# Kernel optimization log

Measured on AMD Instinct MI355X. Metric: run time of the kernel, lower is better.

## Reference

```python
import jax, jax.numpy as jnp
import numpy as np

N_NODES = 50000
N_EDGES = 800000
NUM_GRAPHS = 256
IN = 128
HID = 256
NUM_CLASSES = 10
EPS = 1e-5


def _glorot(key, shape):
    fan_in, fan_out = shape[0], shape[1]
    lim = (6.0 / (fan_in + fan_out)) ** 0.5
    return jax.random.uniform(key, shape, jnp.float32, -lim, lim)


def setup_inputs() -> dict:
    key = jax.random.key(0)
    ks = jax.random.split(key, 32)
    x = jax.random.normal(ks[0], (N_NODES, IN), jnp.float32)
    edge_index = jax.random.randint(ks[1], (2, N_EDGES), 0, N_NODES, jnp.int64)
    batch = jnp.sort(jax.random.randint(ks[2], (N_NODES,), 0, NUM_GRAPHS, jnp.int64))
    h = IN // 2  # 64
    p = {
        "x": x, "edge_index": edge_index, "batch": batch,
        # SAGEConv: out = lin_l(mean_aggr(x_j)) + lin_r(x_i); lin_l has bias, lin_r none
        "W1l": _glorot(ks[3], (IN, h)), "b1l": jnp.zeros((h,), jnp.float32), "W1r": _glorot(ks[4], (IN, h)),
        "W2l": _glorot(ks[5], (h, h)), "b2l": jnp.zeros((h,), jnp.float32), "W2r": _glorot(ks[6], (h, h)),
        "W3l": _glorot(ks[7], (h, h)), "b3l": jnp.zeros((h,), jnp.float32), "W3r": _glorot(ks[8], (h, h)),
        "lin1_w": _glorot(ks[9], (h, HID)), "lin1_b": jnp.zeros((HID,), jnp.float32),
        "g1": jnp.ones((HID,), jnp.float32), "be1": jnp.zeros((HID,), jnp.float32),
        "lin2_w": _glorot(ks[10], (HID, HID // 2)), "lin2_b": jnp.zeros((HID // 2,), jnp.float32),
        "g2": jnp.ones((HID // 2,), jnp.float32), "be2": jnp.zeros((HID // 2,), jnp.float32),
        "lin3_w": _glorot(ks[11], (HID // 2, HID // 4)), "lin3_b": jnp.zeros((HID // 4,), jnp.float32),
        "g3": jnp.ones((HID // 4,), jnp.float32), "be3": jnp.zeros((HID // 4,), jnp.float32),
        "lin4_w": _glorot(ks[12], (HID // 4, NUM_CLASSES)), "lin4_b": jnp.zeros((NUM_CLASSES,), jnp.float32),
    }
    return p


def sage_conv(x, src, dst, Wl, bl, Wr):
    # mean aggregation of source-node messages at destination nodes
    msg = x[src]  # [E, d] gather
    agg = jax.ops.segment_sum(msg, dst, num_segments=N_NODES)
    cnt = jax.ops.segment_sum(jnp.ones((src.shape[0],), x.dtype), dst, num_segments=N_NODES)
    agg = agg / jnp.maximum(cnt, 1.0)[:, None]
    return agg @ Wl + bl + x @ Wr


def batch_norm(x, gamma, beta):
    # training-mode BN (batch statistics, biased variance) as in torch default
    mean = jnp.mean(x, axis=0)
    var = jnp.mean((x - mean) ** 2, axis=0)
    return (x - mean) / jnp.sqrt(var + EPS) * gamma + beta


def reference(x, edge_index, batch,
              W1l, b1l, W1r, W2l, b2l, W2r, W3l, b3l, W3r,
              lin1_w, lin1_b, g1, be1, lin2_w, lin2_b, g2, be2,
              lin3_w, lin3_b, g3, be3, lin4_w, lin4_b):
    src, dst = edge_index[0], edge_index[1]
    h = sage_conv(x, src, dst, W1l, b1l, W1r)
    h = sage_conv(h, src, dst, W2l, b2l, W2r)
    h = sage_conv(h, src, dst, W3l, b3l, W3r)
    # global_mean_pool over graphs
    s = jax.ops.segment_sum(h, batch, num_segments=NUM_GRAPHS)
    n = jax.ops.segment_sum(jnp.ones((h.shape[0],), h.dtype), batch, num_segments=NUM_GRAPHS)
    c = s / jnp.maximum(n, 1.0)[:, None]
    # dropout is identity (self.training = False)
    c = jnp.tanh(batch_norm(c @ lin1_w + lin1_b, g1, be1))
    c = jnp.tanh(batch_norm(c @ lin2_w + lin2_b, g2, be2))
    c = jnp.tanh(batch_norm(c @ lin3_w + lin3_b, g3, be3))
    return c @ lin4_w + lin4_b
```

## Files before the change

### kernel.cpp

```cpp
#include <hip/hip_runtime.h>
#include <hip/hip_bf16.h>

#define N_NODES   50000
#define N_EDGES   800000
#define NUM_GRAPHS 256
#define IN_DIM    128
#define HD        64
#define EPS       1e-5f
#define SCAN_NB   196
#define NB_HEAD   64

typedef __hip_bfloat16 bf16;

__global__ void k_diag(float* __restrict__ out, int n, float v) {
    int t = blockIdx.x * 256 + threadIdx.x;
    if (t < n) out[t] = v;
}

__global__ void k_count(const int* __restrict__ dst, const int* __restrict__ batch,
                        int* __restrict__ cnti, int* __restrict__ pos,
                        int* __restrict__ gb) {
    int e = blockIdx.x * 256 + threadIdx.x;
    if (e < N_EDGES) pos[e] = atomicAdd(&cnti[dst[e]], 1);
    if (e < N_NODES) {
        int bg = batch[e];
        int bnext = (e + 1 < N_NODES) ? batch[e + 1] : NUM_GRAPHS;
        if (e == 0) {
            for (int g = 0; g <= bg; ++g) gb[g] = 0;
        }
        for (int g = bg + 1; g <= bnext; ++g) gb[g] = e + 1;
    }
}

__global__ void k_scan1(const int* __restrict__ cnti, int* __restrict__ off,
                        int* __restrict__ bsum) {
    __shared__ int wsum[4];
    int idx = blockIdx.x * 256 + threadIdx.x;
    int lane = threadIdx.x & 63, wid = threadIdx.x >> 6;
    int v = (idx < N_NODES) ? cnti[idx] : 0;
    int s = v;
    #pragma unroll
    for (int o = 1; o < 64; o <<= 1) {
        int u = __shfl_up(s, o);
        if (lane >= o) s += u;
    }
    if (lane == 63) wsum[wid] = s;
    __syncthreads();
    int wbase = 0;
    #pragma unroll
    for (int w = 0; w < 4; w++) wbase += (w < wid) ? wsum[w] : 0;
    if (idx < N_NODES) off[idx] = wbase + s - v;
    if (threadIdx.x == 255) bsum[blockIdx.x] = wbase + s;
}

__global__ void k_scan3(int* __restrict__ off, const int* __restrict__ bsum,
                        const int* __restrict__ gb, float* __restrict__ invc) {
    __shared__ int wsum[4];
    __shared__ int spre;
    int lane = threadIdx.x & 63, wid = threadIdx.x >> 6;
    int v = (threadIdx.x < blockIdx.x) ? bsum[threadIdx.x] : 0;
    #pragma unroll
    for (int o = 32; o > 0; o >>= 1) v += __shfl_down(v, o);
    if (lane == 0) wsum[wid] = v;
    __syncthreads();
    if (threadIdx.x == 0) spre = wsum[0] + wsum[1] + wsum[2] + wsum[3];
    __syncthreads();
    int pre = spre;
    int idx = blockIdx.x * 256 + threadIdx.x;
    if (idx < N_NODES) off[idx] += pre;
    else if (idx == N_NODES) off[N_NODES] = N_EDGES;
    if (blockIdx.x == 0 && threadIdx.x < NUM_GRAPHS) {
        int c0 = gb[threadIdx.x], c1 = gb[threadIdx.x + 1];
        invc[threadIdx.x] = 1.0f / (float)max(c1 - c0, 1);
    }
}

__global__ void k_fill(const int* __restrict__ src, const int* __restrict__ dst,
                       const int* __restrict__ off, const int* __restrict__ pos,
                       int* __restrict__ nbr, int2* __restrict__ bounds) {
    int e = blockIdx.x * 256 + threadIdx.x;
    if (e < N_NODES) bounds[e] = make_int2(off[e], off[e + 1]);
    if (e >= N_EDGES) return;
    int d = dst[e];
    nbr[off[d] + pos[e]] = src[e];
}

template <int K, int NB>
__global__ __launch_bounds__(256) void k_xform3(
        const float* __restrict__ X, const float* __restrict__ Wl,
        const float* __restrict__ Wr, const float* __restrict__ bl,
        bf16* __restrict__ B, float* __restrict__ C) {
    __shared__ float tile[NB * K];
    const int NPW = NB / 4;
    int nodes0 = blockIdx.x * NB;
    {
        const int total4 = NB * K / 4;
        int nmax4 = (N_NODES - nodes0) * K / 4;
        const float4* Xg = (const float4*)(X + (long)nodes0 * K);
        float4* tg = (float4*)tile;
        for (int idx = threadIdx.x; idx < total4; idx += 256) {
            float4 v = make_float4(0.f, 0.f, 0.f, 0.f);
            if (idx < nmax4) v = Xg[idx];
            tg[idx] = v;
        }
    }
    __syncthreads();
    int wave = threadIdx.x >> 6, j = threadIdx.x & 63;
    long base = (long)nodes0 + wave * NPW;
    if (base >= N_NODES) return;
    float accB[NPW], accC[NPW];
    #pragma unroll
    for (int n = 0; n < NPW; n++) { accB[n] = 0.f; accC[n] = 0.f; }
    const float* Xs = tile + (wave * NPW) * K;
    for (int kc = 0; kc < K; kc += 4) {
        float wl0 = Wl[(kc + 0) * HD + j], wr0 = Wr[(kc + 0) * HD + j];
        float wl1 = Wl[(kc + 1) * HD + j], wr1 = Wr[(kc + 1) * HD + j];
        float wl2 = Wl[(kc + 2) * HD + j], wr2 = Wr[(kc + 2) * HD + j];
        float wl3 = Wl[(kc + 3) * HD + j], wr3 = Wr[(kc + 3) * HD + j];
        #pragma unroll
        for (int n = 0; n < NPW; n++) {
            float4 xv = *(const float4*)(Xs + n * K + kc);
            accB[n] = fmaf(xv.x, wl0, accB[n]);
            accC[n] = fmaf(xv.x, wr0, accC[n]);
            accB[n] = fmaf(xv.y, wl1, accB[n]);
            accC[n] = fmaf(xv.y, wr1, accC[n]);
            accB[n] = fmaf(xv.z, wl2, accB[n]);
            accC[n] = fmaf(xv.z, wr2, accC[n]);
            accB[n] = fmaf(xv.w, wl3, accB[n]);
            accC[n] = fmaf(xv.w, wr3, accC[n]);
        }
    }
    float bb = bl[j];
    int nact = (int)min((long)NPW, (long)N_NODES - base);
    for (int n = 0; n < nact; n++) {
        long i = base + n;
        B[i * HD + j] = __float2bfloat16(accB[n]);
        C[i * HD + j] = accC[n] + bb;
    }
}

__device__ __forceinline__ float bflo(unsigned u) { return __uint_as_float(u << 16); }
__device__ __forceinline__ float bfhi(unsigned u) { return __uint_as_float(u & 0xffff0000u); }

template <bool LAST>
__global__ void k_gather(const int2* __restrict__ bounds, const int* __restrict__ nbr,
                         const bf16* __restrict__ Bm, float* __restrict__ C,
                         const int* __restrict__ batch, const float* __restrict__ invc,
                         float* __restrict__ cb) {
    int t = blockIdx.x * 256 + threadIdx.x;
    int i = t >> 6, lane = t & 63;
    if (!LAST && i >= N_NODES) return;
    int q = lane >> 4, c2 = lane & 15;
    int wid = threadIdx.x >> 6;
    const uint2* B2 = (const uint2*)Bm;
    int2 be = bounds[i];
    int beg = be.x, end = be.y;
    float4 a0 = make_float4(0.f, 0.f, 0.f, 0.f);
    float4 a1 = make_float4(0.f, 0.f, 0.f, 0.f);
    float4 a2 = make_float4(0.f, 0.f, 0.f, 0.f);
    float4 a3 = make_float4(0.f, 0.f, 0.f, 0.f);
    for (int base = beg; base < end; base += 64) {
        int idx = base + lane;
        int nv = (idx < end) ? nbr[idx] : 0;
        int m = min(64, end - base);
        int tt = 0;
        for (; tt + 16 <= m; tt += 16) {
            int n0 = __shfl(nv, tt + 0 + q);
            int n1 = __shfl(nv, tt + 4 + q);
            int n2 = __shfl(nv, tt + 8 + q);
            int n3 = __shfl(nv, tt + 12 + q);
            uint2 u0 = B2[(long)n0 * 16 + c2];
            uint2 u1 = B2[(long)n1 * 16 + c2];
            uint2 u2 = B2[(long)n2 * 16 + c2];
            uint2 u3 = B2[(long)n3 * 16 + c2];
            a0.x += bflo(u0.x); a0.y += bfhi(u0.x); a0.z += bflo(u0.y); a0.w += bfhi(u0.y);
            a1.x += bflo(u1.x); a1.y += bfhi(u1.x); a1.z += bflo(u1.y); a1.w += bfhi(u1.y);
            a2.x += bflo(u2.x); a2.y += bfhi(u2.x); a2.z += bflo(u2.y); a2.w += bfhi(u2.y);
            a3.x += bflo(u3.x); a3.y += bfhi(u3.x); a3.z += bflo(u3.y); a3.w += bfhi(u3.y);
        }
        for (; tt < m; tt += 4) {
            int n0 = __shfl(nv, tt + q);
            if (tt + q < m) {
                uint2 u0 = B2[(long)n0 * 16 + c2];
                a0.x += bflo(u0.x); a0.y += bfhi(u0.x);
                a0.z += bflo(u0.y); a0.w += bfhi(u0.y);
            }
        }
    }
    float4 s;
    s.x = (a0.x + a1.x) + (a2.x + a3.x);
    s.y = (a0.y + a1.y) + (a2.y + a3.y);
    s.z = (a0.z + a1.z) + (a2.z + a3.z);
    s.w = (a0.w + a1.w) + (a2.w + a3.w);
    s.x += __shfl_xor(s.x, 16); s.x += __shfl_xor(s.x, 32);
    s.y += __shfl_xor(s.y, 16); s.y += __shfl_xor(s.y, 32);
    s.z += __shfl_xor(s.z, 16); s.z += __shfl_xor(s.z, 32);
    s.w += __shfl_xor(s.w, 16); s.w += __shfl_xor(s.w, 32);
    if (!LAST) {
        if (lane < 16) {
            int deg = end - beg;
            float inv = 1.0f / (float)max(deg, 1);
            float4* Cp = (float4*)(C + (long)i * HD + 4 * lane);
            float4 cur = *Cp;
            cur.x += s.x * inv;
            cur.y += s.y * inv;
            cur.z += s.z * inv;
            cur.w += s.w * inv;
            *Cp = cur;
        }
    } else {
        __shared__ float red[4][64];
        __shared__ int gid[4];
        if (lane < 16) {
            int deg = end - beg;
            float inv = 1.0f / (float)max(deg, 1);
            const float4 cur = *(const float4*)(C + (long)i * HD + 4 * lane);
            red[wid][4 * lane + 0] = cur.x + s.x * inv;
            red[wid][4 * lane + 1] = cur.y + s.y * inv;
            red[wid][4 * lane + 2] = cur.z + s.z * inv;
            red[wid][4 * lane + 3] = cur.w + s.w * inv;
        }
        if (lane == 0) gid[wid] = batch[i];
        __syncthreads();
        if (wid == 0) {
            int g0 = gid[0], g1 = gid[1], g2 = gid[2], g3 = gid[3];
            float v0 = red[0][lane], v1 = red[1][lane];
            float v2 = red[2][lane], v3 = red[3][lane];
            if (g0 == g3) {
                atomicAdd(&cb[g0 * HD + lane],
                          ((v0 + v1) + (v2 + v3)) * invc[g0]);
            } else {
                atomicAdd(&cb[g0 * HD + lane], v0 * invc[g0]);
                atomicAdd(&cb[g1 * HD + lane], v1 * invc[g1]);
                atomicAdd(&cb[g2 * HD + lane], v2 * invc[g2]);
                atomicAdd(&cb[g3 * HD + lane], v3 * invc[g3]);
            }
        }
    }
}

__device__ __forceinline__ void gbar(int* bar, int round) {
    __syncthreads();
    if (threadIdx.x == 0) {
        __hip_atomic_fetch_add(bar, 1, __ATOMIC_ACQ_REL, __HIP_MEMORY_SCOPE_AGENT);
        int target = round * NB_HEAD;
        while (__hip_atomic_load(bar, __ATOMIC_ACQUIRE, __HIP_MEMORY_SCOPE_AGENT) < target) {}
    }
    __syncthreads();
}

__device__ __forceinline__ float ag_load(const float* p) {
    return __hip_atomic_load(p, __ATOMIC_RELAXED, __HIP_MEMORY_SCOPE_AGENT);
}

template <int NF>
__device__ __forceinline__ void stage4(float* __restrict__ s, const float* __restrict__ g) {
    const float4* g4 = (const float4*)g;
    float4* s4 = (float4*)s;
    #pragma unroll
    for (int i = 0; i < NF / 1024; i++)
        s4[i * 256 + threadIdx.x] = g4[i * 256 + threadIdx.x];
}

__global__ __launch_bounds__(256) void k_head(
        int* bar, float* __restrict__ gstat,
        const float* __restrict__ l1w, const float* __restrict__ l1b,
        const float* __restrict__ g1, const float* __restrict__ be1,
        const float* __restrict__ l2w, const float* __restrict__ l2b,
        const float* __restrict__ g2, const float* __restrict__ be2,
        const float* __restrict__ l3w, const float* __restrict__ l3b,
        const float* __restrict__ g3, const float* __restrict__ be3,
        const float* __restrict__ w4, const float* __restrict__ b4,
        const float* __restrict__ cb, float* __restrict__ out) {
    __shared__ float WB[32768];
    __shared__ float A1[4][64];
    __shared__ float A2[4][256];
    __shared__ float A3[4][128];
    __shared__ float M3[4][64];
    __shared__ float W4[640];
    float* gs1 = gstat;
    float* gq1 = gstat + 256;
    float* gs2 = gstat + 512;
    float* gq2 = gstat + 640;
    float* gs3 = gstat + 768;
    float* gq3 = gstat + 832;
    int t = threadIdx.x;
    int r0 = blockIdx.x * 4;

    {
        int r = t >> 6, lane = t & 63;
        A1[r][lane] = cb[(r0 + r) * HD + lane];
    }
    if (t < 160) ((float4*)W4)[t] = ((const float4*)w4)[t];
    stage4<16384>(WB + 16384, l1w);
    __syncthreads();

    float v1[4];
    {
        float bj = l1b[t];
        v1[0] = bj; v1[1] = bj; v1[2] = bj; v1[3] = bj;
        const float* Wp = WB + 16384;
        #pragma unroll 16
        for (int k = 0; k < 64; k++) {
            float w = Wp[k * 256 + t];
            v1[0] = fmaf(A1[0][k], w, v1[0]);
            v1[1] = fmaf(A1[1][k], w, v1[1]);
            v1[2] = fmaf(A1[2][k], w, v1[2]);
            v1[3] = fmaf(A1[3][k], w, v1[3]);
        }
        float s = (v1[0] + v1[1]) + (v1[2] + v1[3]);
        float q = (v1[0] * v1[0] + v1[1] * v1[1]) + (v1[2] * v1[2] + v1[3] * v1[3]);
        atomicAdd(&gs1[t], s);
        atomicAdd(&gq1[t], q);
    }
    __syncthreads();
    stage4<32768>(WB, l2w);
    gbar(bar, 1);
    {
        float S = ag_load(&gs1[t]), Q = ag_load(&gq1[t]);
        float mean = S * (1.0f / NUM_GRAPHS);
        float var = Q * (1.0f / NUM_GRAPHS) - mean * mean;
        float sc = rsqrtf(fmaxf(var, 0.f) + EPS) * g1[t];
        float sh = be1[t];
        #pragma unroll
        for (int r = 0; r < 4; r++)
            A2[r][t] = tanhf((v1[r] - mean) * sc + sh);
    }
    __syncthreads();

    float v2[2];
    int j2 = t & 127, rq2 = t >> 7;
    {
        float bj = l2b[j2];
        v2[0] = bj; v2[1] = bj;
        const float* a0 = A2[2 * rq2 + 0];
        const float* a1 = A2[2 * rq2 + 1];
        #pragma unroll 16
        for (int k = 0; k < 256; k++) {
            float w = WB[k * 128 + j2];
            v2[0] = fmaf(a0[k], w, v2[0]);
            v2[1] = fmaf(a1[k], w, v2[1]);
        }
        atomicAdd(&gs2[j2], v2[0] + v2[1]);
        atomicAdd(&gq2[j2], v2[0] * v2[0] + v2[1] * v2[1]);
    }
    __syncthreads();
    stage4<8192>(WB, l3w);
    gbar(bar, 2);
    {
        float S = ag_load(&gs2[j2]), Q = ag_load(&gq2[j2]);
        float mean = S * (1.0f / NUM_GRAPHS);
        float var = Q * (1.0f / NUM_GRAPHS) - mean * mean;
        float sc = rsqrtf(fmaxf(var, 0.f) + EPS) * g2[j2];
        float sh = be2[j2];
        A3[2 * rq2 + 0][j2] = tanhf((v2[0] - mean) * sc + sh);
        A3[2 * rq2 + 1][j2] = tanhf((v2[1] - mean) * sc + sh);
    }
    __syncthreads();

    float v3;
    int j3 = t & 63, rq3 = t >> 6;
    {
        float bj = l3b[j3];
        v3 = bj;
        const float* a = A3[rq3];
        #pragma unroll 16
        for (int k = 0; k < 128; k++) {
            float w = WB[k * 64 + j3];
            v3 = fmaf(a[k], w, v3);
        }
        atomicAdd(&gs3[j3], v3);
        atomicAdd(&gq3[j3], v3 * v3);
    }
    gbar(bar, 3);
    {
        float S = ag_load(&gs3[j3]), Q = ag_load(&gq3[j3]);
        float mean = S * (1.0f / NUM_GRAPHS);
        float var = Q * (1.0f / NUM_GRAPHS) - mean * mean;
        float sc = rsqrtf(fmaxf(var, 0.f) + EPS) * g3[j3];
        float sh = be3[j3];
        M3[rq3][j3] = tanhf((v3 - mean) * sc + sh);
    }
    __syncthreads();

    if (t < 40) {
        int q = t / 10, jf = t % 10;
        const float* rp = M3[q];
        float s = b4[jf];
        #pragma unroll
        for (int k = 0; k < 64; k++) s = fmaf(rp[k], W4[k * 10 + jf], s);
        out[(r0 + q) * 10 + jf] = s;
    }
}

extern "C" void kernel_launch(void* const* d_in, const int* in_sizes, int n_in,
                              void* d_out, int out_size, void* d_ws, size_t ws_size,
                              hipStream_t stream) {
    const float* x     = (const float*)d_in[0];
    const int*   ei    = (const int*) d_in[1];
    const int*   batch = (const int*) d_in[2];
    const float *W1l = (const float*)d_in[3],  *b1l = (const float*)d_in[4],  *W1r = (const float*)d_in[5];
    const float *W2l = (const float*)d_in[6],  *b2l = (const float*)d_in[7],  *W2r = (const float*)d_in[8];
    const float *W3l = (const float*)d_in[9],  *b3l = (const float*)d_in[10], *W3r = (const float*)d_in[11];
    const float *lin1_w = (const float*)d_in[12], *lin1_b = (const float*)d_in[13];
    const float *g1 = (const float*)d_in[14], *be1 = (const float*)d_in[15];
    const float *lin2_w = (const float*)d_in[16], *lin2_b = (const float*)d_in[17];
    const float *g2 = (const float*)d_in[18], *be2 = (const float*)d_in[19];
    const float *lin3_w = (const float*)d_in[20], *lin3_b = (const float*)d_in[21];
    const float *g3 = (const float*)d_in[22], *be3 = (const float*)d_in[23];
    const float *lin4_w = (const float*)d_in[24], *lin4_b = (const float*)d_in[25];

    const int* srcp = ei;
    const int* dstp = ei + N_EDGES;

    const long NF = (long)N_NODES * HD;
    char* wsb  = (char*)d_ws;
    int*  cnti = (int*)wsb;
    int*  bar  = cnti + 50048;
    float* gstat = (float*)(bar + 8);
    int*  pos  = (int*)(gstat + 896);
    int*  off  = pos  + 800000;
    int*  nbr  = off  + 50056;
    int*  bsum = nbr  + 800000;
    int*  gb   = bsum + 256;
    float* invc = (float*)(gb + 264);
    int2* bounds = (int2*)(invc + 256);
    bf16* B    = (bf16*)(bounds + 50000);
    float* H1  = (float*)(B + NF);
    float* H2  = H1  + NF;
    float* cb  = H2  + NF;
    float* endp= cb  + NUM_GRAPHS * HD;

    const size_t NEED = (size_t)((char*)endp - wsb);
    if (ws_size < NEED) {
        k_diag<<<(out_size + 255) / 256, 256, 0, stream>>>((float*)d_out, out_size,
                                                           (float)(ws_size >> 20));
        return;
    }

    const int TB = 256;
    const int gNE = (N_EDGES + TB - 1) / TB;
    const int gNF = (int)((NF + TB - 1) / TB);
    const int gX16 = (N_NODES + 15) / 16;

    hipMemsetAsync(cnti, 0, (50048 + 8 + 896) * sizeof(int), stream);
    hipMemsetAsync(cb, 0, NUM_GRAPHS * HD * sizeof(float), stream);

    k_count<<<gNE, TB, 0, stream>>>(dstp, batch, cnti, pos, gb);
    k_scan1<<<SCAN_NB, TB, 0, stream>>>(cnti, off, bsum);
    k_scan3<<<SCAN_NB, TB, 0, stream>>>(off, bsum, gb, invc);
    k_fill<<<gNE, TB, 0, stream>>>(srcp, dstp, off, pos, nbr, bounds);

    k_xform3<IN_DIM, 16><<<gX16, TB, 0, stream>>>(x, W1l, W1r, b1l, B, H1);
    k_gather<false><<<gNF, TB, 0, stream>>>(bounds, nbr, B, H1, batch, invc, cb);
    k_xform3<HD, 16><<<gX16, TB, 0, stream>>>(H1, W2l, W2r, b2l, B, H2);
    k_gather<false><<<gNF, TB, 0, stream>>>(bounds, nbr, B, H2, batch, invc, cb);
    k_xform3<HD, 16><<<gX16, TB, 0, stream>>>(H2, W3l, W3r, b3l, B, H1);
    k_gather<true><<<gNF, TB, 0, stream>>>(bounds, nbr, B, H1, batch, invc, cb);

    k_head<<<NB_HEAD, TB, 0, stream>>>(bar, gstat,
                                       lin1_w, lin1_b, g1, be1,
                                       lin2_w, lin2_b, g2, be2,
                                       lin3_w, lin3_b, g3, be3,
                                       lin4_w, lin4_b,
                                       cb, (float*)d_out);
}
```

Before: 363.8 us.

## Split gather feature dimension into two halves across separate block sets

The neighbor-gather kernel now launches twice as many blocks, each handling one 32-column half of the 64-wide bf16 feature row. Each wave processes 8 neighbors at a time with 8 lanes per 64-byte half-row instead of 4 neighbors with 16 lanes. The aim is more memory-level parallelism per wave and more waves in flight. In exchange, the neighbor index list and bounds are read twice, every 128-byte row is fetched as two 64-byte segments by different blocks, and the pooled atomics are split by column half.

After: 398.7 us. +9.6%, slower.

```diff
diff --git a/kernel.cpp b/kernel.cpp
--- a/kernel.cpp
+++ b/kernel.cpp
@@ -9,6 +9,7 @@
 #define EPS       1e-5f
 #define SCAN_NB   196
 #define NB_HEAD   64
+#define GATHER_NB 12500
 
 typedef __hip_bfloat16 bf16;
 
@@ -143,16 +144,18 @@
 __device__ __forceinline__ float bfhi(unsigned u) { return __uint_as_float(u & 0xffff0000u); }
 
 template <bool LAST>
-__global__ void k_gather(const int2* __restrict__ bounds, const int* __restrict__ nbr,
-                         const bf16* __restrict__ Bm, float* __restrict__ C,
-                         const int* __restrict__ batch, const float* __restrict__ invc,
-                         float* __restrict__ cb) {
-    int t = blockIdx.x * 256 + threadIdx.x;
-    int i = t >> 6, lane = t & 63;
-    if (!LAST && i >= N_NODES) return;
-    int q = lane >> 4, c2 = lane & 15;
-    int wid = threadIdx.x >> 6;
+__global__ __launch_bounds__(256) void k_gather(
+        const int2* __restrict__ bounds, const int* __restrict__ nbr,
+        const bf16* __restrict__ Bm, float* __restrict__ C,
+        const int* __restrict__ batch, const float* __restrict__ invc,
+        float* __restrict__ cb) {
+    int h = blockIdx.x / GATHER_NB;
+    int nb = blockIdx.x % GATHER_NB;
+    int wid = threadIdx.x >> 6, lane = threadIdx.x & 63;
+    int i = nb * 4 + wid;
+    int q = lane >> 3, c = lane & 7;
     const uint2* B2 = (const uint2*)Bm;
+    const long hb = (long)h * 8 + c;
     int2 be = bounds[i];
     int beg = be.x, end = be.y;
     float4 a0 = make_float4(0.f, 0.f, 0.f, 0.f);
@@ -164,24 +167,32 @@
         int nv = (idx < end) ? nbr[idx] : 0;
         int m = min(64, end - base);
         int tt = 0;
-        for (; tt + 16 <= m; tt += 16) {
-            int n0 = __shfl(nv, tt + 0 + q);
-            int n1 = __shfl(nv, tt + 4 + q);
-            int n2 = __shfl(nv, tt + 8 + q);
-            int n3 = __shfl(nv, tt + 12 + q);
-            uint2 u0 = B2[(long)n0 * 16 + c2];
-            uint2 u1 = B2[(long)n1 * 16 + c2];
-            uint2 u2 = B2[(long)n2 * 16 + c2];
-            uint2 u3 = B2[(long)n3 * 16 + c2];
+        for (; tt + 32 <= m; tt += 32) {
+            int n0 = __shfl(nv, tt + q);
+            int n1 = __shfl(nv, tt + 8 + q);
+            int n2 = __shfl(nv, tt + 16 + q);
+            int n3 = __shfl(nv, tt + 24 + q);
+            uint2 u0 = B2[(long)n0 * 16 + hb];
+            uint2 u1 = B2[(long)n1 * 16 + hb];
+            uint2 u2 = B2[(long)n2 * 16 + hb];
+            uint2 u3 = B2[(long)n3 * 16 + hb];
             a0.x += bflo(u0.x); a0.y += bfhi(u0.x); a0.z += bflo(u0.y); a0.w += bfhi(u0.y);
             a1.x += bflo(u1.x); a1.y += bfhi(u1.x); a1.z += bflo(u1.y); a1.w += bfhi(u1.y);
             a2.x += bflo(u2.x); a2.y += bfhi(u2.x); a2.z += bflo(u2.y); a2.w += bfhi(u2.y);
             a3.x += bflo(u3.x); a3.y += bfhi(u3.x); a3.z += bflo(u3.y); a3.w += bfhi(u3.y);
         }
-        for (; tt < m; tt += 4) {
+        for (; tt + 16 <= m; tt += 16) {
+            int n0 = __shfl(nv, tt + q);
+            int n1 = __shfl(nv, tt + 8 + q);
+            uint2 u0 = B2[(long)n0 * 16 + hb];
+            uint2 u1 = B2[(long)n1 * 16 + hb];
+            a0.x += bflo(u0.x); a0.y += bfhi(u0.x); a0.z += bflo(u0.y); a0.w += bfhi(u0.y);
+            a1.x += bflo(u1.x); a1.y += bfhi(u1.x); a1.z += bflo(u1.y); a1.w += bfhi(u1.y);
+        }
+        for (; tt < m; tt += 8) {
             int n0 = __shfl(nv, tt + q);
             if (tt + q < m) {
-                uint2 u0 = B2[(long)n0 * 16 + c2];
+                uint2 u0 = B2[(long)n0 * 16 + hb];
                 a0.x += bflo(u0.x); a0.y += bfhi(u0.x);
                 a0.z += bflo(u0.y); a0.w += bfhi(u0.y);
             }
@@ -192,15 +203,15 @@
     s.y = (a0.y + a1.y) + (a2.y + a3.y);
     s.z = (a0.z + a1.z) + (a2.z + a3.z);
     s.w = (a0.w + a1.w) + (a2.w + a3.w);
-    s.x += __shfl_xor(s.x, 16); s.x += __shfl_xor(s.x, 32);
-    s.y += __shfl_xor(s.y, 16); s.y += __shfl_xor(s.y, 32);
-    s.z += __shfl_xor(s.z, 16); s.z += __shfl_xor(s.z, 32);
-    s.w += __shfl_xor(s.w, 16); s.w += __shfl_xor(s.w, 32);
+    s.x += __shfl_xor(s.x, 8); s.x += __shfl_xor(s.x, 16); s.x += __shfl_xor(s.x, 32);
+    s.y += __shfl_xor(s.y, 8); s.y += __shfl_xor(s.y, 16); s.y += __shfl_xor(s.y, 32);
+    s.z += __shfl_xor(s.z, 8); s.z += __shfl_xor(s.z, 16); s.z += __shfl_xor(s.z, 32);
+    s.w += __shfl_xor(s.w, 8); s.w += __shfl_xor(s.w, 16); s.w += __shfl_xor(s.w, 32);
+    int deg = end - beg;
+    float inv = 1.0f / (float)max(deg, 1);
     if (!LAST) {
-        if (lane < 16) {
-            int deg = end - beg;
-            float inv = 1.0f / (float)max(deg, 1);
-            float4* Cp = (float4*)(C + (long)i * HD + 4 * lane);
+        if (lane < 8) {
+            float4* Cp = (float4*)(C + (long)i * HD + h * 32 + 4 * lane);
             float4 cur = *Cp;
             cur.x += s.x * inv;
             cur.y += s.y * inv;
@@ -209,12 +220,10 @@
             *Cp = cur;
         }
     } else {
-        __shared__ float red[4][64];
+        __shared__ float red[4][32];
         __shared__ int gid[4];
-        if (lane < 16) {
-            int deg = end - beg;
-            float inv = 1.0f / (float)max(deg, 1);
-            const float4 cur = *(const float4*)(C + (long)i * HD + 4 * lane);
+        if (lane < 8) {
+            const float4 cur = *(const float4*)(C + (long)i * HD + h * 32 + 4 * lane);
             red[wid][4 * lane + 0] = cur.x + s.x * inv;
             red[wid][4 * lane + 1] = cur.y + s.y * inv;
             red[wid][4 * lane + 2] = cur.z + s.z * inv;
@@ -222,18 +231,19 @@
         }
         if (lane == 0) gid[wid] = batch[i];
         __syncthreads();
-        if (wid == 0) {
+        if (wid == 0 && lane < 32) {
             int g0 = gid[0], g1 = gid[1], g2 = gid[2], g3 = gid[3];
             float v0 = red[0][lane], v1 = red[1][lane];
             float v2 = red[2][lane], v3 = red[3][lane];
+            int col = h * 32 + lane;
             if (g0 == g3) {
-                atomicAdd(&cb[g0 * HD + lane],
+                atomicAdd(&cb[g0 * HD + col],
                           ((v0 + v1) + (v2 + v3)) * invc[g0]);
             } else {
-                atomicAdd(&cb[g0 * HD + lane], v0 * invc[g0]);
-                atomicAdd(&cb[g1 * HD + lane], v1 * invc[g1]);
-                atomicAdd(&cb[g2 * HD + lane], v2 * invc[g2]);
-                atomicAdd(&cb[g3 * HD + lane], v3 * invc[g3]);
+                atomicAdd(&cb[g0 * HD + col], v0 * invc[g0]);
+                atomicAdd(&cb[g1 * HD + col], v1 * invc[g1]);
+                atomicAdd(&cb[g2 * HD + col], v2 * invc[g2]);
+                atomicAdd(&cb[g3 * HD + col], v3 * invc[g3]);
             }
         }
     }
@@ -440,8 +450,8 @@
 
     const int TB = 256;
     const int gNE = (N_EDGES + TB - 1) / TB;
-    const int gNF = (int)((NF + TB - 1) / TB);
     const int gX16 = (N_NODES + 15) / 16;
+    const int gGA = 2 * GATHER_NB;
 
     hipMemsetAsync(cnti, 0, (50048 + 8 + 896) * sizeof(int), stream);
     hipMemsetAsync(cb, 0, NUM_GRAPHS * HD * sizeof(float), stream);
@@ -452,11 +462,11 @@
     k_fill<<<gNE, TB, 0, stream>>>(srcp, dstp, off, pos, nbr, bounds);
 
     k_xform3<IN_DIM, 16><<<gX16, TB, 0, stream>>>(x, W1l, W1r, b1l, B, H1);
-    k_gather<false><<<gNF, TB, 0, stream>>>(bounds, nbr, B, H1, batch, invc, cb);
+    k_gather<false><<<gGA, TB, 0, stream>>>(bounds, nbr, B, H1, batch, invc, cb);
     k_xform3<HD, 16><<<gX16, TB, 0, stream>>>(H1, W2l, W2r, b2l, B, H2);
-    k_gather<false><<<gNF, TB, 0, stream>>>(bounds, nbr, B, H2, batch, invc, cb);
+    k_gather<false><<<gGA, TB, 0, stream>>>(bounds, nbr, B, H2, batch, invc, cb);
     k_xform3<HD, 16><<<gX16, TB, 0, stream>>>(H2, W3l, W3r, b3l, B, H1);
-    k_gather<true><<<gNF, TB, 0, stream>>>(bounds, nbr, B, H1, batch, invc, cb);
+    k_gather<true><<<gGA, TB, 0, stream>>>(bounds, nbr, B, H1, batch, invc, cb);
 
     k_head<<<NB_HEAD, TB, 0, stream>>>(bar, gstat,
                                        lin1_w, lin1_b, g1, be1,
```
